# Kernel optimization log

Hardware: AMD Instinct MI355X
Metric: run time of the kernel (lower is better)

## Reference

```python
import jax, jax.numpy as jnp
import numpy as np

H, DH = 8, 64          # num_heads, dim_heads
B, N, D = 1, 4096, 512  # batch, seq, model dim
M, CD = 256, 768        # context len, context dim
J = N + 1 + M           # kv length: self + null + context


def _ln(x, scale, bias, eps=1e-6):
    mu = x.mean(-1, keepdims=True)
    var = ((x - mu) ** 2).mean(-1, keepdims=True)
    return (x - mu) * jax.lax.rsqrt(var + eps) * scale + bias


def setup_inputs() -> dict:
    key = jax.random.key(0)
    ks = jax.random.split(key, 8)
    return {
        'x': jax.random.normal(ks[0], (B, N, D), jnp.float32),
        'context': jax.random.normal(ks[1], (B, M, CD), jnp.float32),
        'attn_bias': jax.random.normal(ks[2], (B, H, N, J), jnp.float32) * 0.02,
        'mask': jnp.ones((B, N + M), dtype=bool),
        'ln1_scale': jnp.ones((D,), jnp.float32),
        'ln1_bias': jnp.zeros((D,), jnp.float32),
        'wq': jax.random.normal(ks[3], (D, H * DH), jnp.float32) * (D ** -0.5),
        'wkv': jax.random.normal(ks[4], (D, 2 * DH), jnp.float32) * (D ** -0.5),
        'null_kv': jax.random.normal(ks[5], (2, DH), jnp.float32),
        'ln_ctx_scale': jnp.ones((CD,), jnp.float32),
        'ln_ctx_bias': jnp.zeros((CD,), jnp.float32),
        'wckv': jax.random.normal(ks[6], (CD, 2 * DH), jnp.float32) * (CD ** -0.5),
        'bckv': jnp.zeros((2 * DH,), jnp.float32),
        'wo': jax.random.normal(ks[7], (H * DH, D), jnp.float32) * ((H * DH) ** -0.5),
        'ln_out_scale': jnp.ones((D,), jnp.float32),
        'ln_out_bias': jnp.zeros((D,), jnp.float32),
    }


def reference(x, context, attn_bias, mask, ln1_scale, ln1_bias, wq, wkv,
              null_kv, ln_ctx_scale, ln_ctx_bias, wckv, bckv, wo,
              ln_out_scale, ln_out_bias):
    b, n, d = x.shape
    scale = DH ** -0.5
    xh = _ln(x, ln1_scale, ln1_bias)
    # multi-query: q has heads, k/v are shared (no head dim)
    q = (xh @ wq).reshape(b, n, H, DH).transpose(0, 2, 1, 3) * scale  # b h n d
    k, v = jnp.split(xh @ wkv, 2, axis=-1)                            # b n d each
    # null kv token appended (per source: concat (k, nk))
    nk = jnp.broadcast_to(null_kv[0], (b, 1, DH))
    nv = jnp.broadcast_to(null_kv[1], (b, 1, DH))
    k = jnp.concatenate((k, nk), axis=-2)
    v = jnp.concatenate((v, nv), axis=-2)
    # cross-attention context kv (Dense with bias)
    ch = _ln(context, ln_ctx_scale, ln_ctx_bias)
    ck, cv = jnp.split(ch @ wckv + bckv, 2, axis=-1)
    k = jnp.concatenate((k, ck), axis=-2)  # b j d, j = n+1+m
    v = jnp.concatenate((v, cv), axis=-2)
    sim = jnp.einsum('bhid,bjd->bhij', q, k) + attn_bias
    # pad mask with True for the extra (null) slot, as in source
    m = jnp.pad(mask, ((0, 0), (1, 0)), constant_values=True)[:, None, None, :]
    sim = jnp.where(m, sim, -jnp.finfo(sim.dtype).max)
    attn = jax.nn.softmax(sim, axis=-1)
    out = jnp.einsum('bhij,bjd->bhid', attn, v)
    out = out.transpose(0, 2, 1, 3).reshape(b, n, H * DH) @ wo
    return _ln(out, ln_out_scale, ln_out_bias)
```

## Files before the change

kernel.cpp:

```cpp
#include <hip/hip_runtime.h>
#include <cstdint>
#include <cstddef>

typedef unsigned short u16;
typedef short s16x8 __attribute__((ext_vector_type(8)));
typedef u16 u16x8 __attribute__((ext_vector_type(8)));
typedef u16 u16x4 __attribute__((ext_vector_type(4)));
typedef float f32x4 __attribute__((ext_vector_type(4)));

#define AS1 __attribute__((address_space(1)))
#define AS3 __attribute__((address_space(3)))

#define HH 8
#define DH 64
#define NN 4096
#define DD 512
#define MM 256
#define CDIM 768
#define JTOT 4353
#define JPAD 4416
#define NJT 69
#define SPLITJ 3
#define TILES_PER_SPLIT 23

static __device__ __forceinline__ u16 f2bf(float f) {
    unsigned int u = __builtin_bit_cast(unsigned int, f);
    u += 0x7FFFu + ((u >> 16) & 1u);
    return (u16)(u >> 16);
}
static __device__ __forceinline__ float bf2f(u16 v) {
    unsigned int u = ((unsigned int)v) << 16;
    return __builtin_bit_cast(float, u);
}

static __device__ __forceinline__ f32x4 mfma16(s16x8 a, s16x8 b, f32x4 c) {
    return __builtin_amdgcn_mfma_f32_16x16x32_bf16(a, b, c, 0, 0, 0);
}

static __device__ __forceinline__ void gload16(const void* g, void* l) {
    __builtin_amdgcn_global_load_lds((const AS1 unsigned int*)g,
                                     (AS3 unsigned int*)l, 16, 0, 0);
}

static __device__ __forceinline__ f32x4 loadf4u(const float* p) {
    f32x4 v;
    __builtin_memcpy(&v, p, 16);
    return v;
}

__global__ __launch_bounds__(256) void prep_all(
    const float* __restrict__ wq, const float* __restrict__ wkv,
    const float* __restrict__ wckv, const float* __restrict__ wo,
    const float* __restrict__ null_kv,
    const float* __restrict__ ctx, const float* __restrict__ lncs,
    const float* __restrict__ lncb,
    u16* __restrict__ Wqkv, u16* __restrict__ Wckv, u16* __restrict__ Wo_,
    u16* __restrict__ Kall, u16* __restrict__ VallT, u16* __restrict__ ch) {
    const int bid = blockIdx.x, tid = threadIdx.x;
    if (bid < 1280) {
        int idx = bid * 256 + tid;
        int n = idx >> 9, k = idx & 511;
        float v = (n < 512) ? wq[(size_t)k * 512 + n] * 0.125f
                            : wkv[(size_t)k * 128 + (n - 512)];
        Wqkv[idx] = f2bf(v);
    } else if (bid < 1664) {
        int idx = (bid - 1280) * 256 + tid;
        int n = idx / 768, k = idx - n * 768;
        Wckv[idx] = f2bf(wckv[(size_t)k * 128 + n]);
    } else if (bid < 2688) {
        int idx = (bid - 1664) * 256 + tid;
        int n = idx >> 9, k = idx & 511;
        Wo_[idx] = f2bf(wo[(size_t)k * 512 + n]);
    } else if (bid == 2688) {
        if (tid < 64) {
            Kall[(size_t)4096 * 64 + tid] = f2bf(null_kv[tid]);
            VallT[(size_t)tid * JPAD + (4096 ^ ((tid & 7) << 3))] = f2bf(null_kv[64 + tid]);
        }
        for (int i = tid; i < (JPAD - JTOT) * 64; i += 256) {
            Kall[(size_t)JTOT * 64 + i] = 0;
            int d = i / (JPAD - JTOT), c = JTOT + i - d * (JPAD - JTOT);
            VallT[(size_t)d * JPAD + ((size_t)c ^ ((d & 7) << 3))] = 0;
        }
    } else {
        int row = (bid - 2689) * 4 + (tid >> 6);
        int lane = tid & 63;
        const float4* xp = (const float4*)(ctx + (size_t)row * 768);
        float4 a = xp[lane], b = xp[64 + lane], c = xp[128 + lane];
        float s = a.x+a.y+a.z+a.w + b.x+b.y+b.z+b.w + c.x+c.y+c.z+c.w;
        float q = a.x*a.x+a.y*a.y+a.z*a.z+a.w*a.w + b.x*b.x+b.y*b.y+b.z*b.z+b.w*b.w
                + c.x*c.x+c.y*c.y+c.z*c.z+c.w*c.w;
        #pragma unroll
        for (int m = 1; m < 64; m <<= 1) { s += __shfl_xor(s, m); q += __shfl_xor(q, m); }
        float mu = s * (1.f / 768.f);
        float var = q * (1.f / 768.f) - mu * mu;
        float rs = rsqrtf(var + 1e-6f);
        const float4* sp = (const float4*)lncs;
        const float4* bp = (const float4*)lncb;
        u16x4* op = (u16x4*)(ch + (size_t)row * 768);
        #pragma unroll
        for (int seg = 0; seg < 3; ++seg) {
            float4 v = (seg == 0) ? a : (seg == 1) ? b : c;
            float4 ss = sp[seg * 64 + lane], bb = bp[seg * 64 + lane];
            u16x4 o;
            o[0] = f2bf((v.x - mu) * rs * ss.x + bb.x);
            o[1] = f2bf((v.y - mu) * rs * ss.y + bb.y);
            o[2] = f2bf((v.z - mu) * rs * ss.z + bb.z);
            o[3] = f2bf((v.w - mu) * rs * ss.w + bb.w);
            op[seg * 64 + lane] = o;
        }
    }
}

__global__ __launch_bounds__(256) void ln512_to_bf16(
    const float* __restrict__ x, const float* __restrict__ sc,
    const float* __restrict__ bi, u16* __restrict__ out) {
    int row = blockIdx.x * 4 + (threadIdx.x >> 6);
    int lane = threadIdx.x & 63;
    const float4* xp = (const float4*)(x + (size_t)row * 512);
    float4 a = xp[lane], b = xp[64 + lane];
    float s = a.x + a.y + a.z + a.w + b.x + b.y + b.z + b.w;
    float q = a.x*a.x + a.y*a.y + a.z*a.z + a.w*a.w
            + b.x*b.x + b.y*b.y + b.z*b.z + b.w*b.w;
    #pragma unroll
    for (int m = 1; m < 64; m <<= 1) { s += __shfl_xor(s, m); q += __shfl_xor(q, m); }
    float mu = s * (1.f / 512.f);
    float var = q * (1.f / 512.f) - mu * mu;
    float rs = rsqrtf(var + 1e-6f);
    const float4* sp = (const float4*)sc;
    const float4* bp = (const float4*)bi;
    float4 s0 = sp[lane], s1 = sp[64 + lane], b0 = bp[lane], b1 = bp[64 + lane];
    u16x4 o0, o1;
    o0[0] = f2bf((a.x - mu) * rs * s0.x + b0.x);
    o0[1] = f2bf((a.y - mu) * rs * s0.y + b0.y);
    o0[2] = f2bf((a.z - mu) * rs * s0.z + b0.z);
    o0[3] = f2bf((a.w - mu) * rs * s0.w + b0.w);
    o1[0] = f2bf((b.x - mu) * rs * s1.x + b1.x);
    o1[1] = f2bf((b.y - mu) * rs * s1.y + b1.y);
    o1[2] = f2bf((b.z - mu) * rs * s1.z + b1.z);
    o1[3] = f2bf((b.w - mu) * rs * s1.w + b1.w);
    u16x4* op = (u16x4*)(out + (size_t)row * 512);
    op[lane] = o0;
    op[64 + lane] = o1;
}

__global__ __launch_bounds__(256) void ln512_to_f32(
    const float* __restrict__ x, const float* __restrict__ sc,
    const float* __restrict__ bi, float* __restrict__ out) {
    int row = blockIdx.x * 4 + (threadIdx.x >> 6);
    int lane = threadIdx.x & 63;
    const float4* xp = (const float4*)(x + (size_t)row * 512);
    float4 a = xp[lane], b = xp[64 + lane];
    float s = a.x + a.y + a.z + a.w + b.x + b.y + b.z + b.w;
    float q = a.x*a.x + a.y*a.y + a.z*a.z + a.w*a.w
            + b.x*b.x + b.y*b.y + b.z*b.z + b.w*b.w;
    #pragma unroll
    for (int m = 1; m < 64; m <<= 1) { s += __shfl_xor(s, m); q += __shfl_xor(q, m); }
    float mu = s * (1.f / 512.f);
    float var = q * (1.f / 512.f) - mu * mu;
    float rs = rsqrtf(var + 1e-6f);
    const float4* sp = (const float4*)sc;
    const float4* bp = (const float4*)bi;
    float4 s0 = sp[lane], s1 = sp[64 + lane], b0 = bp[lane], b1 = bp[64 + lane];
    float4 o0, o1;
    o0.x = (a.x - mu) * rs * s0.x + b0.x;
    o0.y = (a.y - mu) * rs * s0.y + b0.y;
    o0.z = (a.z - mu) * rs * s0.z + b0.z;
    o0.w = (a.w - mu) * rs * s0.w + b0.w;
    o1.x = (b.x - mu) * rs * s1.x + b1.x;
    o1.y = (b.y - mu) * rs * s1.y + b1.y;
    o1.z = (b.z - mu) * rs * s1.z + b1.z;
    o1.w = (b.w - mu) * rs * s1.w + b1.w;
    float4* op = (float4*)(out + (size_t)row * 512);
    op[lane] = o0;
    op[64 + lane] = o1;
}

__global__ __launch_bounds__(256) void gemm_bf16(
    const u16* __restrict__ A, int lda, const u16* __restrict__ Bt, int ldb,
    int M, int N, int K, int mode, const float* __restrict__ bias128,
    u16* __restrict__ outQ, u16* __restrict__ outK, u16* __restrict__ outV,
    float* __restrict__ outF) {
    __shared__ __align__(16) u16 Al[128 * 32];
    __shared__ __align__(16) u16 Bl[64 * 32];
    const int tid = threadIdx.x, wave = tid >> 6, lane = tid & 63;
    const int l16 = lane & 15, l4 = lane >> 4;
    const int m0 = blockIdx.x * 128, n0 = blockIdx.y * 64;

    f32x4 acc[2][4] = {};
    const int ms = tid >> 2, ks = (tid & 3) * 8;

    for (int k0 = 0; k0 < K; k0 += 32) {
        __syncthreads();
        gload16(A + (size_t)(m0 + ms) * lda + (k0 + ks), (char*)Al + wave * 1024);
        gload16(A + (size_t)(m0 + 64 + ms) * lda + (k0 + ks), (char*)Al + 4096 + wave * 1024);
        gload16(Bt + (size_t)(n0 + ms) * ldb + (k0 + ks), (char*)Bl + wave * 1024);
        __syncthreads();
        s16x8 af[2], bf[4];
        #pragma unroll
        for (int mf = 0; mf < 2; ++mf)
            af[mf] = *(const s16x8*)&Al[(wave * 32 + mf * 16 + l16) * 32 + l4 * 8];
        #pragma unroll
        for (int nf = 0; nf < 4; ++nf)
            bf[nf] = *(const s16x8*)&Bl[(nf * 16 + l16) * 32 + l4 * 8];
        #pragma unroll
        for (int mf = 0; mf < 2; ++mf)
            #pragma unroll
            for (int nf = 0; nf < 4; ++nf)
                acc[mf][nf] = mfma16(af[mf], bf[nf], acc[mf][nf]);
    }

    #pragma unroll
    for (int mf = 0; mf < 2; ++mf)
        #pragma unroll
        for (int nf = 0; nf < 4; ++nf)
            #pragma unroll
            for (int r = 0; r < 4; ++r) {
                float v = acc[mf][nf][r];
                int m = m0 + wave * 32 + mf * 16 + l4 * 4 + r;
                int n = n0 + nf * 16 + l16;
                if (mode == 0) {
                    if (n < 512) {
                        outQ[(size_t)m * 512 + n] = f2bf(v);
                    } else if (n < 576) {
                        int d = n - 512;
                        outK[(size_t)m * 64 + (d ^ ((m & 7) << 3))] = f2bf(v);
                    } else {
                        int d = n - 576;
                        outV[(size_t)d * JPAD + ((size_t)m ^ ((d & 7) << 3))] = f2bf(v);
                    }
                } else if (mode == 1) {
                    v += bias128[n];
                    int j = 4097 + m;
                    if (n < 64) {
                        outK[(size_t)j * 64 + (n ^ ((j & 7) << 3))] = f2bf(v);
                    } else {
                        int d = n - 64;
                        outV[(size_t)d * JPAD + ((size_t)j ^ ((d & 7) << 3))] = f2bf(v);
                    }
                } else {
                    outF[(size_t)m * 512 + n] = v;
                }
            }
}

__global__ __launch_bounds__(256, 3) void attn_fwd(
    const u16* __restrict__ Q, const u16* __restrict__ Kall,
    const u16* __restrict__ VallT, const float* __restrict__ bias,
    u16* __restrict__ Opart, float* __restrict__ ml) {
    __shared__ __align__(16) u16 Kl[2][64 * 64];
    __shared__ __align__(16) u16 Vl[2][64 * 64];
    __shared__ __align__(16) u16 Pl[4][32][72];

    const int tid = threadIdx.x, wave = tid >> 6, lane = tid & 63;
    const int l16 = lane & 15, l4 = lane >> 4;
    const int qb = blockIdx.x, h = blockIdx.y, sp = blockIdx.z;
    const int tbeg = sp * TILES_PER_SPLIT;
    const int tend = tbeg + TILES_PER_SPLIT;
    const int iw = qb * 128 + wave * 32;

    s16x8 qf[2][2];
    #pragma unroll
    for (int qg = 0; qg < 2; ++qg) {
        const u16* qp = Q + (size_t)(iw + qg * 16 + l16) * 512 + h * 64 + l4 * 8;
        qf[qg][0] = *(const s16x8*)qp;
        qf[qg][1] = *(const s16x8*)(qp + 32);
    }

    f32x4 po[2][4] = {};
    float mrow[2] = {-3.0e38f, -3.0e38f};
    float lrow[2] = {0.f, 0.f};

    const int xsw = (l16 & 7) << 3;
    const int c0 = (l4 * 8) ^ xsw;
    const int c1 = (l4 * 8 + 32) ^ xsw;

    const float* brow0 = bias + ((size_t)h * NN + iw + l16) * JTOT;
    const float* brow1 = brow0 + (size_t)16 * JTOT;

    f32x4 bc[2][4];

#define STAGE_KV(BUF, JT) do { \
        const u16* gk_ = Kall + (size_t)(JT) * 4096 + tid * 8; \
        gload16(gk_,        (char*)Kl[BUF] + wave * 1024); \
        gload16(gk_ + 2048, (char*)Kl[BUF] + 4096 + wave * 1024); \
        const u16* gv_ = VallT + (size_t)(tid >> 3) * JPAD + (size_t)(JT) * 64 + (tid & 7) * 8; \
        gload16(gv_,                     (char*)Vl[BUF] + wave * 1024); \
        gload16(gv_ + (size_t)32 * JPAD, (char*)Vl[BUF] + 4096 + wave * 1024); \
    } while (0)

#define LOAD_BIAS(JT) do { \
        if ((JT) == NJT - 1) { \
            _Pragma("unroll") \
            for (int js_ = 0; js_ < 4; ++js_) { \
                int cb_ = (JT) * 64 + js_ * 16 + l4 * 4; \
                _Pragma("unroll") \
                for (int r_ = 0; r_ < 4; ++r_) { \
                    bool v_ = (cb_ + r_) < JTOT; \
                    bc[0][js_][r_] = v_ ? brow0[cb_ + r_] : 0.f; \
                    bc[1][js_][r_] = v_ ? brow1[cb_ + r_] : 0.f; \
                } \
            } \
        } else { \
            _Pragma("unroll") \
            for (int js_ = 0; js_ < 4; ++js_) { \
                int cb_ = (JT) * 64 + js_ * 16 + l4 * 4; \
                bc[0][js_] = loadf4u(brow0 + cb_); \
                bc[1][js_] = loadf4u(brow1 + cb_); \
            } \
        } \
    } while (0)

#define PIPE_BARRIER() do { \
        asm volatile("s_waitcnt vmcnt(8)" ::: "memory"); \
        __builtin_amdgcn_s_barrier(); \
        __builtin_amdgcn_sched_barrier(0); \
    } while (0)

    STAGE_KV(0, tbeg);
    LOAD_BIAS(tbeg);
    PIPE_BARRIER();

    for (int jt = tbeg; jt < tend; ++jt) {
        const int buf = (jt - tbeg) & 1;
        if (jt + 1 < tend) STAGE_KV(buf ^ 1, jt + 1);
        const u16* kb = &Kl[buf][0];
        const u16* vb = &Vl[buf][0];

        f32x4 s[2][4];
        __builtin_amdgcn_s_setprio(1);
        #pragma unroll
        for (int js = 0; js < 4; ++js) {
            const int ro = (js * 16 + l16) * 64;
            s16x8 kf0 = *(const s16x8*)&kb[ro + c0];
            s16x8 kf1 = *(const s16x8*)&kb[ro + c1];
            #pragma unroll
            for (int qg = 0; qg < 2; ++qg) {
                f32x4 z = {};
                z = mfma16(kf0, qf[qg][0], z);
                z = mfma16(kf1, qf[qg][1], z);
                s[qg][js] = z;
            }
        }
        __builtin_amdgcn_s_setprio(0);
        #pragma unroll
        for (int qg = 0; qg < 2; ++qg)
            #pragma unroll
            for (int js = 0; js < 4; ++js)
                s[qg][js] += bc[qg][js];
        if (jt == NJT - 1) {
            #pragma unroll
            for (int js = 0; js < 4; ++js)
                #pragma unroll
                for (int r = 0; r < 4; ++r)
                    if (jt * 64 + js * 16 + l4 * 4 + r >= JTOT) {
                        s[0][js][r] = -3.0e38f;
                        s[1][js][r] = -3.0e38f;
                    }
        }
        if (jt + 1 < tend) LOAD_BIAS(jt + 1);

        #pragma unroll
        for (int qg = 0; qg < 2; ++qg) {
            float t = s[qg][0][0];
            #pragma unroll
            for (int js = 0; js < 4; ++js)
                #pragma unroll
                for (int r = 0; r < 4; ++r)
                    t = fmaxf(t, s[qg][js][r]);
            t = fmaxf(t, __shfl_xor(t, 16));
            t = fmaxf(t, __shfl_xor(t, 32));
            float mnew = fmaxf(mrow[qg], t);
            float alpha = __expf(mrow[qg] - mnew);
            mrow[qg] = mnew;
            float sum = 0.f;
            #pragma unroll
            for (int js = 0; js < 4; ++js)
                #pragma unroll
                for (int r = 0; r < 4; ++r) {
                    float e = __expf(s[qg][js][r] - mnew);
                    s[qg][js][r] = e;
                    sum += e;
                }
            sum += __shfl_xor(sum, 16);
            sum += __shfl_xor(sum, 32);
            lrow[qg] = lrow[qg] * alpha + sum;
            #pragma unroll
            for (int df = 0; df < 4; ++df)
                #pragma unroll
                for (int r = 0; r < 4; ++r)
                    po[qg][df][r] *= alpha;
            #pragma unroll
            for (int js = 0; js < 4; ++js) {
                u16x4 pk;
                pk[0] = f2bf(s[qg][js][0]);
                pk[1] = f2bf(s[qg][js][1]);
                pk[2] = f2bf(s[qg][js][2]);
                pk[3] = f2bf(s[qg][js][3]);
                *(u16x4*)&Pl[wave][qg * 16 + l16][js * 16 + l4 * 4] = pk;
            }
        }
        s16x8 pf[2][2];
        #pragma unroll
        for (int qg = 0; qg < 2; ++qg) {
            pf[qg][0] = *(const s16x8*)&Pl[wave][qg * 16 + l16][l4 * 8];
            pf[qg][1] = *(const s16x8*)&Pl[wave][qg * 16 + l16][32 + l4 * 8];
        }
        __builtin_amdgcn_s_setprio(1);
        #pragma unroll
        for (int df = 0; df < 4; ++df) {
            const int vo = (df * 16 + l16) * 64;
            s16x8 vf0 = *(const s16x8*)&vb[vo + c0];
            s16x8 vf1 = *(const s16x8*)&vb[vo + c1];
            #pragma unroll
            for (int qg = 0; qg < 2; ++qg) {
                po[qg][df] = mfma16(vf0, pf[qg][0], po[qg][df]);
                po[qg][df] = mfma16(vf1, pf[qg][1], po[qg][df]);
            }
        }
        __builtin_amdgcn_s_setprio(0);
        PIPE_BARRIER();
    }

    const size_t obase = (((size_t)sp * 32 + qb) * 8 + h) * 8192;
    #pragma unroll
    for (int qg = 0; qg < 2; ++qg) {
        const int qlocal = wave * 32 + qg * 16 + l16;
        #pragma unroll
        for (int df = 0; df < 4; ++df) {
            u16x4 pk;
            pk[0] = f2bf(po[qg][df][0]);
            pk[1] = f2bf(po[qg][df][1]);
            pk[2] = f2bf(po[qg][df][2]);
            pk[3] = f2bf(po[qg][df][3]);
            *(u16x4*)&Opart[obase + (size_t)qlocal * 64 + df * 16 + l4 * 4] = pk;
        }
    }
    const size_t mbase = (((size_t)sp * 32 + qb) * 8 + h) * 256;
    if (l4 == 0) {
        #pragma unroll
        for (int qg = 0; qg < 2; ++qg) {
            const int qlocal = wave * 32 + qg * 16 + l16;
            ml[mbase + qlocal] = mrow[qg];
            ml[mbase + 128 + qlocal] = lrow[qg];
        }
    }
#undef STAGE_KV
#undef LOAD_BIAS
#undef PIPE_BARRIER
}

__global__ __launch_bounds__(256) void attn_combine(
    const u16* __restrict__ Opart, const float* __restrict__ ml,
    u16* __restrict__ Ob) {
    const int qb = blockIdx.x, h = blockIdx.y;
    const int t = threadIdx.x;
    const int row = t >> 1, dh = (t & 1) * 32;

    float m[SPLITJ], l[SPLITJ];
    #pragma unroll
    for (int s = 0; s < SPLITJ; ++s) {
        const float* mlp = ml + (((size_t)s * 32 + qb) * 8 + h) * 256;
        m[s] = mlp[row];
        l[s] = mlp[128 + row];
    }
    float mstar = m[0];
    #pragma unroll
    for (int s = 1; s < SPLITJ; ++s) mstar = fmaxf(mstar, m[s]);

    float osum[32] = {};
    float lsum = 0.f;
    #pragma unroll
    for (int s = 0; s < SPLITJ; ++s) {
        float w = __expf(m[s] - mstar);
        lsum += w * l[s];
        const u16* op = Opart + (((size_t)s * 32 + qb) * 8 + h) * 8192
                        + (size_t)row * 64 + dh;
        #pragma unroll
        for (int c = 0; c < 4; ++c) {
            u16x8 a = *(const u16x8*)(op + c * 8);
            #pragma unroll
            for (int e = 0; e < 8; ++e)
                osum[c * 8 + e] += w * bf2f(a[e]);
        }
    }
    float inv = 1.f / lsum;
    u16* dst = Ob + (size_t)(qb * 128 + row) * 512 + h * 64 + dh;
    #pragma unroll
    for (int c = 0; c < 4; ++c) {
        u16x8 o;
        #pragma unroll
        for (int e = 0; e < 8; ++e) o[e] = f2bf(osum[c * 8 + e] * inv);
        *(u16x8*)(dst + c * 8) = o;
    }
}

extern "C" void kernel_launch(void* const* d_in, const int* in_sizes, int n_in,
                              void* d_out, int out_size, void* d_ws, size_t ws_size,
                              hipStream_t stream) {
    (void)in_sizes; (void)n_in; (void)out_size; (void)ws_size;
    const float* x     = (const float*)d_in[0];
    const float* ctx   = (const float*)d_in[1];
    const float* bias  = (const float*)d_in[2];
    const float* ln1s  = (const float*)d_in[4];
    const float* ln1b  = (const float*)d_in[5];
    const float* wq    = (const float*)d_in[6];
    const float* wkv   = (const float*)d_in[7];
    const float* nullkv= (const float*)d_in[8];
    const float* lncs  = (const float*)d_in[9];
    const float* lncb  = (const float*)d_in[10];
    const float* wckv  = (const float*)d_in[11];
    const float* bckv  = (const float*)d_in[12];
    const float* wo    = (const float*)d_in[13];
    const float* lnos  = (const float*)d_in[14];
    const float* lnob  = (const float*)d_in[15];
    float* out = (float*)d_out;

    char* ws = (char*)d_ws;
    u16*   Wo_   = (u16*)(ws + 0);
    u16*   Wqkv  = (u16*)(ws + 524288);
    float* Ml    = (float*)(ws + 524288);
    u16*   Wckv  = (u16*)(ws + 1179648);
    u16*   ch    = (u16*)(ws + 1572864);
    u16*   Qb    = (u16*)(ws + 1966080);
    u16*   Ob    = (u16*)(ws + 1966080);
    u16*   Kall  = (u16*)(ws + 6160384);
    u16*   VallT = (u16*)(ws + 6725632);
    u16*   xh    = (u16*)(ws + 7290880);
    u16*   Opart = (u16*)(ws + 7290880);
    float* tmp   = (float*)(ws + 7290880);

    prep_all<<<2753, 256, 0, stream>>>(wq, wkv, wckv, wo, nullkv, ctx, lncs, lncb,
                                       Wqkv, Wckv, Wo_, Kall, VallT, ch);
    ln512_to_bf16<<<1024, 256, 0, stream>>>(x, ln1s, ln1b, xh);
    gemm_bf16<<<dim3(32, 10), 256, 0, stream>>>(xh, 512, Wqkv, 512, 4096, 640, 512,
                                                0, nullptr, Qb, Kall, VallT, nullptr);
    gemm_bf16<<<dim3(2, 2), 256, 0, stream>>>(ch, 768, Wckv, 768, 256, 128, 768,
                                              1, bckv, nullptr, Kall, VallT, nullptr);
    attn_fwd<<<dim3(32, 8, SPLITJ), 256, 0, stream>>>(Qb, Kall, VallT, bias, Opart, Ml);
    attn_combine<<<dim3(32, 8), 256, 0, stream>>>(Opart, Ml, Ob);
    gemm_bf16<<<dim3(32, 8), 256, 0, stream>>>(Ob, 512, Wo_, 512, 4096, 512, 512,
                                               2, nullptr, nullptr, nullptr, nullptr, tmp);
    ln512_to_f32<<<1024, 256, 0, stream>>>(tmp, lnos, lnob, out);
}
```

Baseline: 234.4 us.

## Unroll attention loop by two, seed scores with bias, read V from global

Restructures the flash-attention inner loop to handle two K tiles per barrier, with two tiles staged in LDS per buffer. The bias tile is loaded straight into the MFMA accumulators so the separate bias add and the out-of-range masking pass go away; padded columns get a large negative bias instead. V fragments are now read directly from global memory into registers rather than staged through LDS. This halves the number of barriers and frees LDS. The trade-off is more register pressure and V reads that depend on cache behaviour rather than coalesced staging.

```diff
diff --git a/kernel.cpp b/kernel.cpp
--- a/kernel.cpp
+++ b/kernel.cpp
@@ -247,8 +247,7 @@
     const u16* __restrict__ Q, const u16* __restrict__ Kall,
     const u16* __restrict__ VallT, const float* __restrict__ bias,
     u16* __restrict__ Opart, float* __restrict__ ml) {
-    __shared__ __align__(16) u16 Kl[2][64 * 64];
-    __shared__ __align__(16) u16 Vl[2][64 * 64];
+    __shared__ __align__(16) u16 KlF[2 * 2 * 4096];
     __shared__ __align__(16) u16 Pl[4][32][72];
 
     const int tid = threadIdx.x, wave = tid >> 6, lane = tid & 63;
@@ -277,18 +276,18 @@
     const float* brow0 = bias + ((size_t)h * NN + iw + l16) * JTOT;
     const float* brow1 = brow0 + (size_t)16 * JTOT;
 
-    f32x4 bc[2][4];
-
-#define STAGE_KV(BUF, JT) do { \
-        const u16* gk_ = Kall + (size_t)(JT) * 4096 + tid * 8; \
-        gload16(gk_,        (char*)Kl[BUF] + wave * 1024); \
-        gload16(gk_ + 2048, (char*)Kl[BUF] + 4096 + wave * 1024); \
-        const u16* gv_ = VallT + (size_t)(tid >> 3) * JPAD + (size_t)(JT) * 64 + (tid & 7) * 8; \
-        gload16(gv_,                     (char*)Vl[BUF] + wave * 1024); \
-        gload16(gv_ + (size_t)32 * JPAD, (char*)Vl[BUF] + 4096 + wave * 1024); \
+    f32x4 sA[2][4], sB[2][4];
+
+#define STAGE_K1(BUF, SLOT, JT) do { \
+        if ((JT) < tend) { \
+            const u16* gk_ = Kall + (size_t)(JT) * 4096 + tid * 8; \
+            char* d_ = (char*)KlF + (BUF) * 16384 + (SLOT) * 8192 + wave * 1024; \
+            gload16(gk_, d_); \
+            gload16(gk_ + 2048, d_ + 4096); \
+        } \
     } while (0)
 
-#define LOAD_BIAS(JT) do { \
+#define LOAD_BIAS_T(SN, JT) do { \
         if ((JT) == NJT - 1) { \
             _Pragma("unroll") \
             for (int js_ = 0; js_ < 4; ++js_) { \
@@ -296,129 +295,138 @@
                 _Pragma("unroll") \
                 for (int r_ = 0; r_ < 4; ++r_) { \
                     bool v_ = (cb_ + r_) < JTOT; \
-                    bc[0][js_][r_] = v_ ? brow0[cb_ + r_] : 0.f; \
-                    bc[1][js_][r_] = v_ ? brow1[cb_ + r_] : 0.f; \
+                    SN[0][js_][r_] = v_ ? brow0[cb_ + r_] : -3.0e38f; \
+                    SN[1][js_][r_] = v_ ? brow1[cb_ + r_] : -3.0e38f; \
                 } \
             } \
         } else { \
             _Pragma("unroll") \
             for (int js_ = 0; js_ < 4; ++js_) { \
                 int cb_ = (JT) * 64 + js_ * 16 + l4 * 4; \
-                bc[0][js_] = loadf4u(brow0 + cb_); \
-                bc[1][js_] = loadf4u(brow1 + cb_); \
+                SN[0][js_] = loadf4u(brow0 + cb_); \
+                SN[1][js_] = loadf4u(brow1 + cb_); \
             } \
         } \
     } while (0)
 
-#define PIPE_BARRIER() do { \
-        asm volatile("s_waitcnt vmcnt(8)" ::: "memory"); \
-        __builtin_amdgcn_s_barrier(); \
-        __builtin_amdgcn_sched_barrier(0); \
+#define VLOAD(VF0, VF1, JT) do { \
+        _Pragma("unroll") \
+        for (int df_ = 0; df_ < 4; ++df_) { \
+            const u16* vp_ = VallT + (size_t)(df_ * 16 + l16) * JPAD + (size_t)(JT) * 64; \
+            VF0[df_] = *(const s16x8*)&vp_[c0]; \
+            VF1[df_] = *(const s16x8*)&vp_[c1]; \
+        } \
     } while (0)
 
-    STAGE_KV(0, tbeg);
-    LOAD_BIAS(tbeg);
-    PIPE_BARRIER();
-
-    for (int jt = tbeg; jt < tend; ++jt) {
-        const int buf = (jt - tbeg) & 1;
-        if (jt + 1 < tend) STAGE_KV(buf ^ 1, jt + 1);
-        const u16* kb = &Kl[buf][0];
-        const u16* vb = &Vl[buf][0];
-
-        f32x4 s[2][4];
-        __builtin_amdgcn_s_setprio(1);
-        #pragma unroll
-        for (int js = 0; js < 4; ++js) {
-            const int ro = (js * 16 + l16) * 64;
-            s16x8 kf0 = *(const s16x8*)&kb[ro + c0];
-            s16x8 kf1 = *(const s16x8*)&kb[ro + c1];
-            #pragma unroll
-            for (int qg = 0; qg < 2; ++qg) {
-                f32x4 z = {};
-                z = mfma16(kf0, qf[qg][0], z);
-                z = mfma16(kf1, qf[qg][1], z);
-                s[qg][js] = z;
-            }
-        }
-        __builtin_amdgcn_s_setprio(0);
-        #pragma unroll
-        for (int qg = 0; qg < 2; ++qg)
-            #pragma unroll
-            for (int js = 0; js < 4; ++js)
-                s[qg][js] += bc[qg][js];
-        if (jt == NJT - 1) {
-            #pragma unroll
-            for (int js = 0; js < 4; ++js)
-                #pragma unroll
-                for (int r = 0; r < 4; ++r)
-                    if (jt * 64 + js * 16 + l4 * 4 + r >= JTOT) {
-                        s[0][js][r] = -3.0e38f;
-                        s[1][js][r] = -3.0e38f;
-                    }
-        }
-        if (jt + 1 < tend) LOAD_BIAS(jt + 1);
-
-        #pragma unroll
-        for (int qg = 0; qg < 2; ++qg) {
-            float t = s[qg][0][0];
-            #pragma unroll
-            for (int js = 0; js < 4; ++js)
-                #pragma unroll
-                for (int r = 0; r < 4; ++r)
-                    t = fmaxf(t, s[qg][js][r]);
-            t = fmaxf(t, __shfl_xor(t, 16));
-            t = fmaxf(t, __shfl_xor(t, 32));
-            float mnew = fmaxf(mrow[qg], t);
-            float alpha = __expf(mrow[qg] - mnew);
-            mrow[qg] = mnew;
-            float sum = 0.f;
-            #pragma unroll
-            for (int js = 0; js < 4; ++js)
-                #pragma unroll
-                for (int r = 0; r < 4; ++r) {
-                    float e = __expf(s[qg][js][r] - mnew);
-                    s[qg][js][r] = e;
-                    sum += e;
-                }
-            sum += __shfl_xor(sum, 16);
-            sum += __shfl_xor(sum, 32);
-            lrow[qg] = lrow[qg] * alpha + sum;
-            #pragma unroll
-            for (int df = 0; df < 4; ++df)
-                #pragma unroll
-                for (int r = 0; r < 4; ++r)
-                    po[qg][df][r] *= alpha;
-            #pragma unroll
-            for (int js = 0; js < 4; ++js) {
-                u16x4 pk;
-                pk[0] = f2bf(s[qg][js][0]);
-                pk[1] = f2bf(s[qg][js][1]);
-                pk[2] = f2bf(s[qg][js][2]);
-                pk[3] = f2bf(s[qg][js][3]);
-                *(u16x4*)&Pl[wave][qg * 16 + l16][js * 16 + l4 * 4] = pk;
-            }
-        }
-        s16x8 pf[2][2];
-        #pragma unroll
-        for (int qg = 0; qg < 2; ++qg) {
-            pf[qg][0] = *(const s16x8*)&Pl[wave][qg * 16 + l16][l4 * 8];
-            pf[qg][1] = *(const s16x8*)&Pl[wave][qg * 16 + l16][32 + l4 * 8];
-        }
-        __builtin_amdgcn_s_setprio(1);
-        #pragma unroll
-        for (int df = 0; df < 4; ++df) {
-            const int vo = (df * 16 + l16) * 64;
-            s16x8 vf0 = *(const s16x8*)&vb[vo + c0];
-            s16x8 vf1 = *(const s16x8*)&vb[vo + c1];
-            #pragma unroll
-            for (int qg = 0; qg < 2; ++qg) {
-                po[qg][df] = mfma16(vf0, pf[qg][0], po[qg][df]);
-                po[qg][df] = mfma16(vf1, pf[qg][1], po[qg][df]);
-            }
-        }
-        __builtin_amdgcn_s_setprio(0);
-        PIPE_BARRIER();
+#define QKT(SC, BUF, SLOT) do { \
+        const u16* kb_ = &KlF[(BUF) * 8192 + (SLOT) * 4096]; \
+        __builtin_amdgcn_s_setprio(1); \
+        _Pragma("unroll") \
+        for (int js_ = 0; js_ < 4; ++js_) { \
+            const int ro_ = (js_ * 16 + l16) * 64; \
+            s16x8 kf0_ = *(const s16x8*)&kb_[ro_ + c0]; \
+            s16x8 kf1_ = *(const s16x8*)&kb_[ro_ + c1]; \
+            _Pragma("unroll") \
+            for (int qg_ = 0; qg_ < 2; ++qg_) { \
+                SC[qg_][js_] = mfma16(kf0_, qf[qg_][0], SC[qg_][js_]); \
+                SC[qg_][js_] = mfma16(kf1_, qf[qg_][1], SC[qg_][js_]); \
+            } \
+        } \
+        __builtin_amdgcn_s_setprio(0); \
+    } while (0)
+
+#define SOFTMAX_P(SC) do { \
+        _Pragma("unroll") \
+        for (int qg_ = 0; qg_ < 2; ++qg_) { \
+            float t_ = SC[qg_][0][0]; \
+            _Pragma("unroll") \
+            for (int js_ = 0; js_ < 4; ++js_) \
+                _Pragma("unroll") \
+                for (int r_ = 0; r_ < 4; ++r_) t_ = fmaxf(t_, SC[qg_][js_][r_]); \
+            t_ = fmaxf(t_, __shfl_xor(t_, 16)); \
+            t_ = fmaxf(t_, __shfl_xor(t_, 32)); \
+            float mnew_ = fmaxf(mrow[qg_], t_); \
+            float alpha_ = __expf(mrow[qg_] - mnew_); \
+            mrow[qg_] = mnew_; \
+            float sum_ = 0.f; \
+            _Pragma("unroll") \
+            for (int js_ = 0; js_ < 4; ++js_) { \
+                u16x4 pk_; \
+                _Pragma("unroll") \
+                for (int r_ = 0; r_ < 4; ++r_) { \
+                    float e_ = __expf(SC[qg_][js_][r_] - mnew_); \
+                    sum_ += e_; \
+                    pk_[r_] = f2bf(e_); \
+                } \
+                *(u16x4*)&Pl[wave][qg_ * 16 + l16][js_ * 16 + l4 * 4] = pk_; \
+            } \
+            sum_ += __shfl_xor(sum_, 16); \
+            sum_ += __shfl_xor(sum_, 32); \
+            lrow[qg_] = lrow[qg_] * alpha_ + sum_; \
+            _Pragma("unroll") \
+            for (int df_ = 0; df_ < 4; ++df_) \
+                _Pragma("unroll") \
+                for (int r_ = 0; r_ < 4; ++r_) po[qg_][df_][r_] *= alpha_; \
+        } \
+    } while (0)
+
+#define PV(VF0, VF1) do { \
+        s16x8 pf_[2][2]; \
+        _Pragma("unroll") \
+        for (int qg_ = 0; qg_ < 2; ++qg_) { \
+            pf_[qg_][0] = *(const s16x8*)&Pl[wave][qg_ * 16 + l16][l4 * 8]; \
+            pf_[qg_][1] = *(const s16x8*)&Pl[wave][qg_ * 16 + l16][32 + l4 * 8]; \
+        } \
+        __builtin_amdgcn_s_setprio(1); \
+        _Pragma("unroll") \
+        for (int df_ = 0; df_ < 4; ++df_) \
+            _Pragma("unroll") \
+            for (int qg_ = 0; qg_ < 2; ++qg_) { \
+                po[qg_][df_] = mfma16(VF0[df_], pf_[qg_][0], po[qg_][df_]); \
+                po[qg_][df_] = mfma16(VF1[df_], pf_[qg_][1], po[qg_][df_]); \
+            } \
+        __builtin_amdgcn_s_setprio(0); \
+    } while (0)
+
+    STAGE_K1(0, 0, tbeg);
+    STAGE_K1(0, 1, tbeg + 1);
+    LOAD_BIAS_T(sA, tbeg);
+    LOAD_BIAS_T(sB, tbeg + 1);
+    asm volatile("s_waitcnt vmcnt(16)" ::: "memory");
+    __builtin_amdgcn_s_barrier();
+    __builtin_amdgcn_sched_barrier(0);
+
+    for (int jt = tbeg; jt + 1 < tend; jt += 2) {
+        const int buf = ((jt - tbeg) >> 1) & 1;
+        STAGE_K1(buf ^ 1, 0, jt + 2);
+        STAGE_K1(buf ^ 1, 1, jt + 3);
+
+        s16x8 vf0[4], vf1[4];
+        VLOAD(vf0, vf1, jt);
+        QKT(sA, buf, 0);
+        SOFTMAX_P(sA);
+        LOAD_BIAS_T(sA, jt + 2);
+        PV(vf0, vf1);
+
+        VLOAD(vf0, vf1, jt + 1);
+        QKT(sB, buf, 1);
+        SOFTMAX_P(sB);
+        if (jt + 3 < tend) LOAD_BIAS_T(sB, jt + 3);
+        PV(vf0, vf1);
+
+        asm volatile("s_waitcnt vmcnt(8)" ::: "memory");
+        __builtin_amdgcn_s_barrier();
+        __builtin_amdgcn_sched_barrier(0);
+    }
+
+    {
+        const int jt = tend - 1;
+        const int buf = ((jt - tbeg) >> 1) & 1;
+        s16x8 vf0[4], vf1[4];
+        VLOAD(vf0, vf1, jt);
+        QKT(sA, buf, 0);
+        SOFTMAX_P(sA);
+        PV(vf0, vf1);
     }
 
     const size_t obase = (((size_t)sp * 32 + qb) * 8 + h) * 8192;
@@ -444,9 +452,12 @@
             ml[mbase + 128 + qlocal] = lrow[qg];
         }
     }
-#undef STAGE_KV
-#undef LOAD_BIAS
-#undef PIPE_BARRIER
+#undef STAGE_K1
+#undef LOAD_BIAS_T
+#undef VLOAD
+#undef QKT
+#undef SOFTMAX_P
+#undef PV
 }
 
 __global__ __launch_bounds__(256) void attn_combine(
```

Result: slower. 425.8 us (+81.7%).
